# Performance work log

Hardware: AMD Instinct MI355X
Metric: run time of the kernel (lower is better)

## Reference

```python
import jax, jax.numpy as jnp
import numpy as np

EPS = 1e-10


def setup_inputs() -> dict:
    key = jax.random.key(0)
    k1, k2 = jax.random.split(key)
    b, p, c = 8192, 512, 1000
    x = jax.random.normal(k1, (b, p), dtype=jnp.float32)
    means = jax.random.normal(k2, (c, p), dtype=jnp.float32)
    return {"x": x, "means": means}


def reference(x, means):
    # scale factor: L2 norm of the first class mean (np.linalg.norm(mean_logits_np[0]))
    scale = jnp.sqrt(jnp.sum(means[0] ** 2))
    # L2-normalize x along feature dim, then rescale to ||means[0]||
    xn = x / (jnp.linalg.norm(x, axis=1, keepdims=True) + EPS) * scale
    # logits = -||xn - mu_c||^2, expanded as -(||xn||^2 - 2 xn.mu + ||mu||^2)
    # avoids materializing the (b, num_classes, p) intermediate of the original
    x_sq = jnp.sum(xn * xn, axis=1, keepdims=True)          # (b, 1)
    m_sq = jnp.sum(means * means, axis=1)                   # (c,)
    cross = jnp.einsum('bp,cp->bc', xn, means)              # (b, c)
    logits = -(x_sq - 2.0 * cross + m_sq[None, :])
    return logits
```

## Files before the change

### kernel.cpp

```cpp
#include <hip/hip_runtime.h>
#include <hip/hip_bf16.h>
#include <stdint.h>

typedef __bf16 bf16x8 __attribute__((ext_vector_type(8)));
typedef float  f32x4  __attribute__((ext_vector_type(4)));
typedef __attribute__((address_space(1))) const void* gptr_t;
typedef __attribute__((address_space(3))) void*       sptr_t;

#define B_ROWS 8192
#define C_CLS  1000
#define C_PAD  1024
#define P_DIM  512
#define EPS    1e-10f

#define WS_MEANS_BF 0
#define WS_MSQ      1048576
#define WS_XN_BF    1052672
#define WS_XSQ      9441280

__device__ __forceinline__ float dot8(float4 a, float4 b) {
    return a.x * a.x + a.y * a.y + a.z * a.z + a.w * a.w
         + b.x * b.x + b.y * b.y + b.z * b.z + b.w * b.w;
}

__global__ __launch_bounds__(256) void prep_k(const float* __restrict__ x,
                                              const float* __restrict__ means,
                                              __hip_bfloat16* __restrict__ means_bf,
                                              float* __restrict__ m_sq,
                                              __hip_bfloat16* __restrict__ xn_bf,
                                              float* __restrict__ x_sq) {
    const int w = threadIdx.x >> 6;
    const int l = threadIdx.x & 63;
    const int bid = blockIdx.x;

    if (bid < B_ROWS / 4) {
        const int row = bid * 4 + w;
        const float4* m0 = (const float4*)means;
        float4 ma = m0[l * 2];
        float4 mb = m0[l * 2 + 1];
        float ms = dot8(ma, mb);
        const float4* xr = (const float4*)(x + (size_t)row * P_DIM);
        float4 a = xr[l * 2];
        float4 b = xr[l * 2 + 1];
        float s = dot8(a, b);
        #pragma unroll
        for (int off = 32; off > 0; off >>= 1) {
            ms += __shfl_down(ms, off);
            s  += __shfl_down(s, off);
        }
        ms = __shfl(ms, 0);
        s  = __shfl(s, 0);
        float scale = sqrtf(ms);
        float norm  = sqrtf(s);
        float sc    = scale / (norm + EPS);
        alignas(16) __hip_bfloat16 tmp[8];
        tmp[0] = __float2bfloat16(a.x * sc); tmp[1] = __float2bfloat16(a.y * sc);
        tmp[2] = __float2bfloat16(a.z * sc); tmp[3] = __float2bfloat16(a.w * sc);
        tmp[4] = __float2bfloat16(b.x * sc); tmp[5] = __float2bfloat16(b.y * sc);
        tmp[6] = __float2bfloat16(b.z * sc); tmp[7] = __float2bfloat16(b.w * sc);
        *(uint4*)(xn_bf + (size_t)row * P_DIM + l * 8) = *(const uint4*)tmp;
        if (l == 0) {
            float sn = sc * norm;
            x_sq[row] = sn * sn;
        }
    } else {
        const int c = (bid - B_ROWS / 4) * 4 + w;
        if (c < C_CLS) {
            const float4* mr = (const float4*)(means + (size_t)c * P_DIM);
            float4 a = mr[l * 2];
            float4 b = mr[l * 2 + 1];
            float s = dot8(a, b);
            alignas(16) __hip_bfloat16 tmp[8];
            tmp[0] = __float2bfloat16(a.x); tmp[1] = __float2bfloat16(a.y);
            tmp[2] = __float2bfloat16(a.z); tmp[3] = __float2bfloat16(a.w);
            tmp[4] = __float2bfloat16(b.x); tmp[5] = __float2bfloat16(b.y);
            tmp[6] = __float2bfloat16(b.z); tmp[7] = __float2bfloat16(b.w);
            *(uint4*)(means_bf + (size_t)c * P_DIM + l * 8) = *(const uint4*)tmp;
            #pragma unroll
            for (int off = 32; off > 0; off >>= 1) s += __shfl_down(s, off);
            if (l == 0) m_sq[c] = s;
        } else {
            uint4 z = {0u, 0u, 0u, 0u};
            *(uint4*)(means_bf + (size_t)c * P_DIM + l * 8) = z;
            if (l == 0) m_sq[c] = 0.0f;
        }
    }
}

__global__ __launch_bounds__(512, 4) void gemm_k(const __hip_bfloat16* __restrict__ A,
                                                 const __hip_bfloat16* __restrict__ B,
                                                 const float* __restrict__ x_sq,
                                                 const float* __restrict__ m_sq,
                                                 float* __restrict__ out) {
    __shared__ alignas(16) char lds[32768];
    const int t   = threadIdx.x;
    const int w   = t >> 6;
    const int l   = t & 63;
    const int q   = l >> 4;
    const int m16 = l & 15;
    const int wr  = w >> 2;
    const int wc  = w & 3;

    const int n_blk  = blockIdx.x;
    const int xcd    = n_blk & 7;
    const int within = n_blk >> 3;
    const int brow   = xcd * 8 + (within & 7);
    const int bcol   = within >> 3;

    f32x4 acc[4][2];
    #pragma unroll
    for (int i = 0; i < 4; ++i)
        #pragma unroll
        for (int j = 0; j < 2; ++j) {
            f32x4 z = {0.f, 0.f, 0.f, 0.f};
            acc[i][j] = z;
        }

    const char* Abase = (const char*)A + (size_t)(brow * 128) * (P_DIM * 2);
    const char* Bbase = (const char*)B + (size_t)(bcol * 128) * (P_DIM * 2);

    const int swz = (m16 & 7) << 4;

    for (int k0 = 0; k0 < P_DIM; k0 += 64) {
        #pragma unroll
        for (int r = 0; r < 4; ++r) {
            const int o   = (r & 1) * 8192 + w * 1024 + l * 16;
            const int row = o >> 7;
            const int c   = (o >> 4) & 7;
            const char* gb = (r < 2) ? Abase : Bbase;
            const char* g  = gb + (size_t)row * (P_DIM * 2) + k0 * 2 + ((c ^ (row & 7)) << 4);
            char* dst = lds + ((r < 2) ? 0 : 16384) + (r & 1) * 8192 + w * 1024;
            __builtin_amdgcn_global_load_lds((gptr_t)g, (sptr_t)dst, 16, 0, 0);
        }
        __syncthreads();

        #pragma unroll
        for (int s = 0; s < 2; ++s) {
            const int kb = s * 64 + q * 16;
            bf16x8 af[4], bfr[2];
            #pragma unroll
            for (int i = 0; i < 4; ++i) {
                const int m = wr * 64 + i * 16 + m16;
                af[i] = *(const bf16x8*)(lds + m * 128 + (kb ^ swz));
            }
            #pragma unroll
            for (int j = 0; j < 2; ++j) {
                const int nn = wc * 32 + j * 16 + m16;
                bfr[j] = *(const bf16x8*)(lds + 16384 + nn * 128 + (kb ^ swz));
            }
            #pragma unroll
            for (int i = 0; i < 4; ++i)
                #pragma unroll
                for (int j = 0; j < 2; ++j)
                    acc[i][j] = __builtin_amdgcn_mfma_f32_16x16x32_bf16(af[i], bfr[j], acc[i][j], 0, 0, 0);
        }
        __syncthreads();
    }

    const int rowbase = brow * 128 + wr * 64;
    const int colbase = bcol * 128 + wc * 32;
    float msq[2];
    #pragma unroll
    for (int j = 0; j < 2; ++j) {
        const int col = colbase + j * 16 + m16;
        msq[j] = (col < C_CLS) ? m_sq[col] : 0.0f;
    }
    #pragma unroll
    for (int i = 0; i < 4; ++i) {
        #pragma unroll
        for (int reg = 0; reg < 4; ++reg) {
            const int row = rowbase + i * 16 + q * 4 + reg;
            const float xsq = x_sq[row];
            #pragma unroll
            for (int j = 0; j < 2; ++j) {
                const int col = colbase + j * 16 + m16;
                if (col < C_CLS) {
                    out[(size_t)row * C_CLS + col] = 2.0f * acc[i][j][reg] - xsq - msq[j];
                }
            }
        }
    }
}

extern "C" void kernel_launch(void* const* d_in, const int* in_sizes, int n_in,
                              void* d_out, int out_size, void* d_ws, size_t ws_size,
                              hipStream_t stream) {
    const float* x     = (const float*)d_in[0];
    const float* means = (const float*)d_in[1];
    float* out = (float*)d_out;
    char* ws = (char*)d_ws;

    __hip_bfloat16* means_bf = (__hip_bfloat16*)(ws + WS_MEANS_BF);
    float*          m_sq     = (float*)(ws + WS_MSQ);
    __hip_bfloat16* xn_bf    = (__hip_bfloat16*)(ws + WS_XN_BF);
    float*          x_sq     = (float*)(ws + WS_XSQ);

    prep_k<<<B_ROWS / 4 + C_PAD / 4, 256, 0, stream>>>(x, means, means_bf, m_sq, xn_bf, x_sq);
    gemm_k<<<512, 512, 0, stream>>>(xn_bf, means_bf, x_sq, m_sq, out);
}
```

Measured before the change: 89.13 us.

## Fuse normalization and bf16 conversion into GEMM, applying row scale in epilogue

Removes the separate prep kernel and workspace round-trip. The GEMM now loads fp32 x and means directly, converts them to bf16 in registers, and writes them into swizzled LDS while accumulating row sums of squares. The per-row normalization scale is applied in the epilogue, since scaling commutes with the dot product. Global loads for the next k-tile are register-prefetched, but each block re-reads fp32 data (twice the bytes) and repeats the conversion work across column tiles instead of using async global-to-LDS loads.

```diff
diff --git a/kernel.cpp b/kernel.cpp
--- a/kernel.cpp
+++ b/kernel.cpp
@@ -4,95 +4,25 @@
 
 typedef __bf16 bf16x8 __attribute__((ext_vector_type(8)));
 typedef float  f32x4  __attribute__((ext_vector_type(4)));
-typedef __attribute__((address_space(1))) const void* gptr_t;
-typedef __attribute__((address_space(3))) void*       sptr_t;
 
 #define B_ROWS 8192
 #define C_CLS  1000
-#define C_PAD  1024
 #define P_DIM  512
 #define EPS    1e-10f
-
-#define WS_MEANS_BF 0
-#define WS_MSQ      1048576
-#define WS_XN_BF    1052672
-#define WS_XSQ      9441280
 
 __device__ __forceinline__ float dot8(float4 a, float4 b) {
     return a.x * a.x + a.y * a.y + a.z * a.z + a.w * a.w
          + b.x * b.x + b.y * b.y + b.z * b.z + b.w * b.w;
 }
 
-__global__ __launch_bounds__(256) void prep_k(const float* __restrict__ x,
-                                              const float* __restrict__ means,
-                                              __hip_bfloat16* __restrict__ means_bf,
-                                              float* __restrict__ m_sq,
-                                              __hip_bfloat16* __restrict__ xn_bf,
-                                              float* __restrict__ x_sq) {
-    const int w = threadIdx.x >> 6;
-    const int l = threadIdx.x & 63;
-    const int bid = blockIdx.x;
+__global__ __launch_bounds__(512, 4) void fused_k(const float* __restrict__ X,
+                                                  const float* __restrict__ M,
+                                                  float* __restrict__ out) {
+    __shared__ alignas(16) char lds[32768];
+    __shared__ float ssq_lds[128];
+    __shared__ float msq_lds[128];
+    __shared__ float scale_lds;
 
-    if (bid < B_ROWS / 4) {
-        const int row = bid * 4 + w;
-        const float4* m0 = (const float4*)means;
-        float4 ma = m0[l * 2];
-        float4 mb = m0[l * 2 + 1];
-        float ms = dot8(ma, mb);
-        const float4* xr = (const float4*)(x + (size_t)row * P_DIM);
-        float4 a = xr[l * 2];
-        float4 b = xr[l * 2 + 1];
-        float s = dot8(a, b);
-        #pragma unroll
-        for (int off = 32; off > 0; off >>= 1) {
-            ms += __shfl_down(ms, off);
-            s  += __shfl_down(s, off);
-        }
-        ms = __shfl(ms, 0);
-        s  = __shfl(s, 0);
-        float scale = sqrtf(ms);
-        float norm  = sqrtf(s);
-        float sc    = scale / (norm + EPS);
-        alignas(16) __hip_bfloat16 tmp[8];
-        tmp[0] = __float2bfloat16(a.x * sc); tmp[1] = __float2bfloat16(a.y * sc);
-        tmp[2] = __float2bfloat16(a.z * sc); tmp[3] = __float2bfloat16(a.w * sc);
-        tmp[4] = __float2bfloat16(b.x * sc); tmp[5] = __float2bfloat16(b.y * sc);
-        tmp[6] = __float2bfloat16(b.z * sc); tmp[7] = __float2bfloat16(b.w * sc);
-        *(uint4*)(xn_bf + (size_t)row * P_DIM + l * 8) = *(const uint4*)tmp;
-        if (l == 0) {
-            float sn = sc * norm;
-            x_sq[row] = sn * sn;
-        }
-    } else {
-        const int c = (bid - B_ROWS / 4) * 4 + w;
-        if (c < C_CLS) {
-            const float4* mr = (const float4*)(means + (size_t)c * P_DIM);
-            float4 a = mr[l * 2];
-            float4 b = mr[l * 2 + 1];
-            float s = dot8(a, b);
-            alignas(16) __hip_bfloat16 tmp[8];
-            tmp[0] = __float2bfloat16(a.x); tmp[1] = __float2bfloat16(a.y);
-            tmp[2] = __float2bfloat16(a.z); tmp[3] = __float2bfloat16(a.w);
-            tmp[4] = __float2bfloat16(b.x); tmp[5] = __float2bfloat16(b.y);
-            tmp[6] = __float2bfloat16(b.z); tmp[7] = __float2bfloat16(b.w);
-            *(uint4*)(means_bf + (size_t)c * P_DIM + l * 8) = *(const uint4*)tmp;
-            #pragma unroll
-            for (int off = 32; off > 0; off >>= 1) s += __shfl_down(s, off);
-            if (l == 0) m_sq[c] = s;
-        } else {
-            uint4 z = {0u, 0u, 0u, 0u};
-            *(uint4*)(means_bf + (size_t)c * P_DIM + l * 8) = z;
-            if (l == 0) m_sq[c] = 0.0f;
-        }
-    }
-}
-
-__global__ __launch_bounds__(512, 4) void gemm_k(const __hip_bfloat16* __restrict__ A,
-                                                 const __hip_bfloat16* __restrict__ B,
-                                                 const float* __restrict__ x_sq,
-                                                 const float* __restrict__ m_sq,
-                                                 float* __restrict__ out) {
-    __shared__ alignas(16) char lds[32768];
     const int t   = threadIdx.x;
     const int w   = t >> 6;
     const int l   = t & 63;
@@ -107,6 +37,19 @@
     const int brow   = xcd * 8 + (within & 7);
     const int bcol   = within >> 3;
 
+    const int prow = t >> 2;
+    const int pseg = t & 3;
+
+    if (w == 0) {
+        const float4* m0 = (const float4*)M;
+        float4 ma = m0[l * 2];
+        float4 mb = m0[l * 2 + 1];
+        float ms = dot8(ma, mb);
+        #pragma unroll
+        for (int off = 32; off > 0; off >>= 1) ms += __shfl_down(ms, off);
+        if (l == 0) scale_lds = sqrtf(ms);
+    }
+
     f32x4 acc[4][2];
     #pragma unroll
     for (int i = 0; i < 4; ++i)
@@ -116,23 +59,69 @@
             acc[i][j] = z;
         }
 
-    const char* Abase = (const char*)A + (size_t)(brow * 128) * (P_DIM * 2);
-    const char* Bbase = (const char*)B + (size_t)(bcol * 128) * (P_DIM * 2);
+    const float* Arow = X + (size_t)(brow * 128 + prow) * P_DIM + pseg * 16;
+    const int    grow = bcol * 128 + prow;
+    const float* Brow = M + (size_t)grow * P_DIM + pseg * 16;
+    const bool   bvalid = (grow < C_CLS);
 
+    const int sc0 = (((pseg * 2)     ^ (prow & 7)) << 4);
+    const int sc1 = (((pseg * 2 + 1) ^ (prow & 7)) << 4);
+    char* const awr = lds + prow * 128;
+    char* const bwr = lds + 16384 + prow * 128;
     const int swz = (m16 & 7) << 4;
 
-    for (int k0 = 0; k0 < P_DIM; k0 += 64) {
-        #pragma unroll
-        for (int r = 0; r < 4; ++r) {
-            const int o   = (r & 1) * 8192 + w * 1024 + l * 16;
-            const int row = o >> 7;
-            const int c   = (o >> 4) & 7;
-            const char* gb = (r < 2) ? Abase : Bbase;
-            const char* g  = gb + (size_t)row * (P_DIM * 2) + k0 * 2 + ((c ^ (row & 7)) << 4);
-            char* dst = lds + ((r < 2) ? 0 : 16384) + (r & 1) * 8192 + w * 1024;
-            __builtin_amdgcn_global_load_lds((gptr_t)g, (sptr_t)dst, 16, 0, 0);
+    float ssqa = 0.f, ssqb = 0.f;
+
+    float4 A0, A1, A2, A3, B0, B1, B2, B3;
+    {
+        const float4* p = (const float4*)Arow;
+        A0 = p[0]; A1 = p[1]; A2 = p[2]; A3 = p[3];
+        float4 z = {0.f, 0.f, 0.f, 0.f};
+        B0 = z; B1 = z; B2 = z; B3 = z;
+        if (bvalid) {
+            const float4* pb = (const float4*)Brow;
+            B0 = pb[0]; B1 = pb[1]; B2 = pb[2]; B3 = pb[3];
+        }
+    }
+
+    for (int kt = 0; kt < 8; ++kt) {
+        ssqa += dot8(A0, A1) + dot8(A2, A3);
+        ssqb += dot8(B0, B1) + dot8(B2, B3);
+        {
+            alignas(16) __hip_bfloat16 ta[16];
+            ta[0]  = __float2bfloat16(A0.x); ta[1]  = __float2bfloat16(A0.y);
+            ta[2]  = __float2bfloat16(A0.z); ta[3]  = __float2bfloat16(A0.w);
+            ta[4]  = __float2bfloat16(A1.x); ta[5]  = __float2bfloat16(A1.y);
+            ta[6]  = __float2bfloat16(A1.z); ta[7]  = __float2bfloat16(A1.w);
+            ta[8]  = __float2bfloat16(A2.x); ta[9]  = __float2bfloat16(A2.y);
+            ta[10] = __float2bfloat16(A2.z); ta[11] = __float2bfloat16(A2.w);
+            ta[12] = __float2bfloat16(A3.x); ta[13] = __float2bfloat16(A3.y);
+            ta[14] = __float2bfloat16(A3.z); ta[15] = __float2bfloat16(A3.w);
+            *(uint4*)(awr + sc0) = ((const uint4*)ta)[0];
+            *(uint4*)(awr + sc1) = ((const uint4*)ta)[1];
+            alignas(16) __hip_bfloat16 tb[16];
+            tb[0]  = __float2bfloat16(B0.x); tb[1]  = __float2bfloat16(B0.y);
+            tb[2]  = __float2bfloat16(B0.z); tb[3]  = __float2bfloat16(B0.w);
+            tb[4]  = __float2bfloat16(B1.x); tb[5]  = __float2bfloat16(B1.y);
+            tb[6]  = __float2bfloat16(B1.z); tb[7]  = __float2bfloat16(B1.w);
+            tb[8]  = __float2bfloat16(B2.x); tb[9]  = __float2bfloat16(B2.y);
+            tb[10] = __float2bfloat16(B2.z); tb[11] = __float2bfloat16(B2.w);
+            tb[12] = __float2bfloat16(B3.x); tb[13] = __float2bfloat16(B3.y);
+            tb[14] = __float2bfloat16(B3.z); tb[15] = __float2bfloat16(B3.w);
+            *(uint4*)(bwr + sc0) = ((const uint4*)tb)[0];
+            *(uint4*)(bwr + sc1) = ((const uint4*)tb)[1];
         }
         __syncthreads();
+
+        if (kt < 7) {
+            const int k0 = (kt + 1) * 64;
+            const float4* p = (const float4*)(Arow + k0);
+            A0 = p[0]; A1 = p[1]; A2 = p[2]; A3 = p[3];
+            if (bvalid) {
+                const float4* pb = (const float4*)(Brow + k0);
+                B0 = pb[0]; B1 = pb[1]; B2 = pb[2]; B3 = pb[3];
+            }
+        }
 
         #pragma unroll
         for (int s = 0; s < 2; ++s) {
@@ -157,25 +146,37 @@
         __syncthreads();
     }
 
+    ssqa += __shfl_xor(ssqa, 1); ssqa += __shfl_xor(ssqa, 2);
+    ssqb += __shfl_xor(ssqb, 1); ssqb += __shfl_xor(ssqb, 2);
+    if (pseg == 0) {
+        ssq_lds[prow] = ssqa;
+        msq_lds[prow] = ssqb;
+    }
+    __syncthreads();
+
+    const float scale = scale_lds;
     const int rowbase = brow * 128 + wr * 64;
     const int colbase = bcol * 128 + wc * 32;
     float msq[2];
     #pragma unroll
     for (int j = 0; j < 2; ++j) {
-        const int col = colbase + j * 16 + m16;
-        msq[j] = (col < C_CLS) ? m_sq[col] : 0.0f;
+        msq[j] = msq_lds[wc * 32 + j * 16 + m16];
     }
     #pragma unroll
     for (int i = 0; i < 4; ++i) {
         #pragma unroll
         for (int reg = 0; reg < 4; ++reg) {
-            const int row = rowbase + i * 16 + q * 4 + reg;
-            const float xsq = x_sq[row];
+            const int lrow = wr * 64 + i * 16 + q * 4 + reg;
+            const int row  = rowbase + i * 16 + q * 4 + reg;
+            const float nrm = sqrtf(ssq_lds[lrow]);
+            const float sc  = scale / (nrm + EPS);
+            const float sn  = sc * nrm;
+            const float xsq = sn * sn;
             #pragma unroll
             for (int j = 0; j < 2; ++j) {
                 const int col = colbase + j * 16 + m16;
                 if (col < C_CLS) {
-                    out[(size_t)row * C_CLS + col] = 2.0f * acc[i][j][reg] - xsq - msq[j];
+                    out[(size_t)row * C_CLS + col] = 2.0f * sc * acc[i][j][reg] - xsq - msq[j];
                 }
             }
         }
@@ -188,13 +189,7 @@
     const float* x     = (const float*)d_in[0];
     const float* means = (const float*)d_in[1];
     float* out = (float*)d_out;
-    char* ws = (char*)d_ws;
+    (void)d_ws; (void)ws_size;
 
-    __hip_bfloat16* means_bf = (__hip_bfloat16*)(ws + WS_MEANS_BF);
-    float*          m_sq     = (float*)(ws + WS_MSQ);
-    __hip_bfloat16* xn_bf    = (__hip_bfloat16*)(ws + WS_XN_BF);
-    float*          x_sq     = (float*)(ws + WS_XSQ);
-
-    prep_k<<<B_ROWS / 4 + C_PAD / 4, 256, 0, stream>>>(x, means, means_bf, m_sq, xn_bf, x_sq);
-    gemm_k<<<512, 512, 0, stream>>>(xn_bf, means_bf, x_sq, m_sq, out);
+    fused_k<<<512, 512, 0, stream>>>(x, means, out);
 }
```

Result: slower. 94.25 us (+5.7%).
